# Optimization experiments

Hardware: AMD Instinct MI355X
Metric: run time of the kernel (lower is better)

Reference implementation:

```python
import jax, jax.numpy as jnp
import numpy as np


def setup_inputs() -> dict:
    key = jax.random.key(0)
    k1, k2, k3 = jax.random.split(key, 3)
    N, C_in, H, W = 32, 64, 128, 128
    C_out, K = 128, 3
    fan_in = C_in * K * K
    bound = 1.0 / np.sqrt(fan_in)
    x = jax.random.normal(k1, (N, C_in, H, W), dtype=jnp.float32)
    weight = jax.random.uniform(k2, (C_out, C_in, K, K), dtype=jnp.float32, minval=-bound, maxval=bound)
    bias = jax.random.uniform(k3, (C_out,), dtype=jnp.float32, minval=-bound, maxval=bound)
    return {"x": x, "weight": weight, "bias": bias}


def reference(x, weight, bias):
    # conv2d, stride=1, padding=0 (VALID), NCHW / OIHW
    y = jax.lax.conv_general_dilated(
        x, weight,
        window_strides=(1, 1),
        padding='VALID',
        dimension_numbers=('NCHW', 'OIHW', 'NCHW'),
    )
    y = y + bias[None, :, None, None]          # [N, C_out, H_out, W_out]
    y = jnp.min(y, axis=1, keepdims=True)      # channel-wise min -> [N, 1, H_out, W_out]
    return jnp.tanh(jnp.tanh(y))
```

## Files before the change

### kernel.cpp

```cpp
#include <hip/hip_runtime.h>
#include <hip/hip_bf16.h>

typedef __attribute__((ext_vector_type(8))) short short8_t;
typedef __attribute__((ext_vector_type(4))) float floatx4;
typedef unsigned short ushort_t;
typedef unsigned int uint_t;

#define RSTR 72
#define TSZ  (132 * RSTR)

__device__ __forceinline__ uint_t rne_u(float f) {
    uint_t u = __float_as_uint(f);
    return u + (0x7fffu + ((u >> 16) & 1u));
}
__device__ __forceinline__ uint_t pk2(float lo, float hi) {
    return __builtin_amdgcn_perm(rne_u(hi), rne_u(lo), 0x07060302u);
}

__global__ void w2_prepass(const float* __restrict__ w, ushort_t* __restrict__ w2) {
    int idx = blockIdx.x * 256 + threadIdx.x;
    int rd  = idx >> 12;
    int rem = idx & 4095;
    int co  = rem >> 5;
    int c32 = rem & 31;
    int khw = rd >> 1, half = rd & 1;
    int ci  = half * 32 + c32;
    w2[idx] = (ushort_t)(rne_u(w[co * 576 + ci * 9 + khw]) >> 16);
}

template<bool USE_W2>
__global__ __launch_bounds__(512, 4)
void conv_min_tanh_kernel(const float* __restrict__ x,
                          const float* __restrict__ w,
                          const ushort_t* __restrict__ w2,
                          const float* __restrict__ bias,
                          float* __restrict__ out)
{
    __shared__ ushort_t T[4 * TSZ];
    __shared__ float red[2][256];

    const int tid  = threadIdx.x;
    const int bid0 = blockIdx.x;
    const int bid  = (bid0 & 7) * 252 + (bid0 >> 3);
    const int n    = bid / 63;
    const int ho0  = (bid - n * 63) * 2;

    const int tx = tid & 31;
    const int ty = tid >> 5;

    const int lane = tid & 63;
    const int wid  = tid >> 6;
    const int wm   = wid >> 1;
    const int wn   = wid & 1;
    const int r16  = lane & 15;
    const int quad = lane >> 4;

    const float* xbase = x + ((size_t)n << 20) + (size_t)ho0 * 128;

    auto load_row = [&](floatx4 (&dv)[4], const int s) {
#pragma unroll
        for (int j = 0; j < 4; ++j)
            dv[j] = *reinterpret_cast<const floatx4*>(
                xbase + (size_t)(ty * 4 + j) * 16384 + s * 128 + tx * 4);
    };
    auto conv_row = [&](floatx4 (&dv)[4], const int s) {
#pragma unroll
        for (int i = 0; i < 4; ++i) {
            uint2 u;
            u.x = pk2(dv[0][i], dv[1][i]);
            u.y = pk2(dv[2][i], dv[3][i]);
            const int c   = tx * 4 + i;
            const int swz = (ty >> 1) ^ ((c >> 3) & 7);
            *reinterpret_cast<uint2*>(&T[s * TSZ + c * RSTR + swz * 8 + (ty & 1) * 4]) = u;
        }
    };

    floatx4 dva[4], dvb[4];
    load_row(dva, 0);
    load_row(dvb, 1);

    for (int idx = tid; idx < 576; idx += 512) {
        int s = idx / 144, o = idx - s * 144;
        reinterpret_cast<uint_t*>(T)[s * (TSZ / 2) + (128 * RSTR) / 2 + o] = 0u;
    }

    conv_row(dva, 0);
    load_row(dva, 2);
    conv_row(dvb, 1);
    load_row(dvb, 3);
    conv_row(dva, 2);
    conv_row(dvb, 3);

    floatx4 acc[4][4];
#pragma unroll
    for (int i = 0; i < 4; ++i)
#pragma unroll
        for (int j = 0; j < 4; ++j)
            acc[i][j] = (floatx4){0.f, 0.f, 0.f, 0.f};

    const ushort_t* w2base = w2 + (size_t)(wn * 64 + r16) * 32 + quad * 8;
    const float*    wbase  = w + (size_t)(wn * 64 + r16) * 576;

    __syncthreads();

#pragma unroll
    for (int rd = 0; rd < 18; ++rd) {
        const int khw  = rd >> 1;
        const int kh   = khw / 3;
        const int kw   = khw - kh * 3;
        const int half = rd & 1;

        short8_t bfr[4];
        if (USE_W2) {
            const ushort_t* bb = w2base + rd * 4096;
#pragma unroll
            for (int t4 = 0; t4 < 4; ++t4)
                bfr[t4] = *reinterpret_cast<const short8_t*>(bb + t4 * 512);
        } else {
#pragma unroll
            for (int t4 = 0; t4 < 4; ++t4) {
                const float* wp = wbase + (size_t)t4 * (16 * 576)
                                + (size_t)(half * 32 + quad * 8) * 9 + khw;
                short8_t b;
#pragma unroll
                for (int q = 0; q < 4; ++q) {
                    uint_t u = pk2(wp[(2 * q) * 9], wp[(2 * q + 1) * 9]);
                    b[2 * q]     = (short)(u & 0xffffu);
                    b[2 * q + 1] = (short)(u >> 16);
                }
                bfr[t4] = b;
            }
        }

        short8_t afr[4];
#pragma unroll
        for (int t4 = 0; t4 < 4; ++t4) {
            const int m  = wm * 64 + t4 * 16 + r16;
            const int s  = (m >> 7) + kh;
            const int c  = (m & 127) + kw;
            const int sw = (half * 4 + quad) ^ ((c >> 3) & 7);
            afr[t4] = *reinterpret_cast<const short8_t*>(&T[s * TSZ + c * RSTR + sw * 8]);
        }
#pragma unroll
        for (int tm = 0; tm < 4; ++tm)
#pragma unroll
            for (int tn = 0; tn < 4; ++tn)
                acc[tm][tn] = __builtin_amdgcn_mfma_f32_16x16x32_bf16(
                    afr[tm], bfr[tn], acc[tm][tn], 0, 0, 0);
    }

    float bvv[4];
#pragma unroll
    for (int tn = 0; tn < 4; ++tn)
        bvv[tn] = bias[wn * 64 + tn * 16 + r16];

#pragma unroll
    for (int tm = 0; tm < 4; ++tm) {
#pragma unroll
        for (int r = 0; r < 4; ++r) {
            float v = acc[tm][0][r] + bvv[0];
            v = fminf(v, acc[tm][1][r] + bvv[1]);
            v = fminf(v, acc[tm][2][r] + bvv[2]);
            v = fminf(v, acc[tm][3][r] + bvv[3]);
            v = fminf(v, __shfl_xor(v, 1, 64));
            v = fminf(v, __shfl_xor(v, 2, 64));
            v = fminf(v, __shfl_xor(v, 4, 64));
            v = fminf(v, __shfl_xor(v, 8, 64));
            if (r16 == 0)
                red[wn][wm * 64 + tm * 16 + quad * 4 + r] = v;
        }
    }
    __syncthreads();

    if (tid < 256) {
        const int r  = tid >> 7;
        const int wo = tid & 127;
        if (wo < 126) {
            float v = fminf(red[0][tid], red[1][tid]);
            v = tanhf(tanhf(v));
            out[((size_t)n * 126 + ho0 + r) * 126 + wo] = v;
        }
    }
}

extern "C" void kernel_launch(void* const* d_in, const int* in_sizes, int n_in,
                              void* d_out, int out_size, void* d_ws, size_t ws_size,
                              hipStream_t stream) {
    const float* x    = (const float*)d_in[0];
    const float* w    = (const float*)d_in[1];
    const float* bias = (const float*)d_in[2];
    float* out = (float*)d_out;

    const int use_w2 = (ws_size >= (size_t)(73728 * 2)) ? 1 : 0;
    ushort_t* w2 = (ushort_t*)d_ws;

    if (use_w2) {
        w2_prepass<<<dim3(288), dim3(256), 0, stream>>>(w, w2);
        conv_min_tanh_kernel<true><<<dim3(2016), dim3(512), 0, stream>>>(x, w, w2, bias, out);
    } else {
        conv_min_tanh_kernel<false><<<dim3(2016), dim3(512), 0, stream>>>(x, w, w2, bias, out);
    }
}
```

Measured before the change: 276.2 us.

## Prepack input to bf16 channels-last and DMA tiles directly into LDS

Adds a prepass that transposes the fp32 NCHW input into a bf16 NHWC workspace buffer. A new conv kernel then loads its LDS tiles with global_load_lds, with no per-thread conversion or swizzled stores. The aim is to remove the fp32 load and pack overhead in the conv prologue. In exchange it adds a full extra pass over the input and a 64MB workspace requirement, and falls back to the old kernel if the workspace is too small.

```diff
diff --git a/kernel.cpp b/kernel.cpp
--- a/kernel.cpp
+++ b/kernel.cpp
@@ -5,6 +5,8 @@
 typedef __attribute__((ext_vector_type(4))) float floatx4;
 typedef unsigned short ushort_t;
 typedef unsigned int uint_t;
+
+#define TILE_B 16896
 
 #define RSTR 72
 #define TSZ  (132 * RSTR)
@@ -28,25 +30,47 @@
     w2[idx] = (ushort_t)(rne_u(w[co * 576 + ci * 9 + khw]) >> 16);
 }
 
-template<bool USE_W2>
+__global__ __launch_bounds__(256)
+void x2_prepass(const float* __restrict__ x, ushort_t* __restrict__ x2) {
+    __shared__ __align__(16) float lds[64 * 129];
+    const int t = threadIdx.x;
+    const int b = blockIdx.x;
+    const int n = b >> 7, h = b & 127;
+    const float* xp = x + ((size_t)n << 20) + (size_t)h * 128;
+#pragma unroll
+    for (int r = 0; r < 32; ++r) {
+        int flat = r * 256 + t;
+        int ci = flat >> 7, wq = flat & 127;
+        lds[ci * 129 + wq] = xp[(size_t)ci * 16384 + wq];
+    }
+    __syncthreads();
+    ushort_t* op = x2 + ((size_t)n * 128 + h) * 128 * 64;
+#pragma unroll
+    for (int r = 0; r < 4; ++r) {
+        int id = r * 256 + t;
+        int wq = id >> 3, q = id & 7;
+        uint_t o[4];
+#pragma unroll
+        for (int qq = 0; qq < 4; ++qq)
+            o[qq] = pk2(lds[(q * 8 + 2 * qq) * 129 + wq],
+                        lds[(q * 8 + 2 * qq + 1) * 129 + wq]);
+        *reinterpret_cast<uint4*>(op + (size_t)wq * 64 + q * 8) =
+            make_uint4(o[0], o[1], o[2], o[3]);
+    }
+}
+
 __global__ __launch_bounds__(512, 4)
-void conv_min_tanh_kernel(const float* __restrict__ x,
-                          const float* __restrict__ w,
-                          const ushort_t* __restrict__ w2,
-                          const float* __restrict__ bias,
-                          float* __restrict__ out)
+void conv_v3(const ushort_t* __restrict__ x2, const ushort_t* __restrict__ w2,
+             const float* __restrict__ bias, float* __restrict__ out)
 {
-    __shared__ ushort_t T[4 * TSZ];
-    __shared__ float red[2][256];
+    __shared__ __align__(16) ushort_t T[4 * (TILE_B / 2)];
+    __shared__ __align__(16) float red[2][256];
 
     const int tid  = threadIdx.x;
     const int bid0 = blockIdx.x;
     const int bid  = (bid0 & 7) * 252 + (bid0 >> 3);
     const int n    = bid / 63;
     const int ho0  = (bid - n * 63) * 2;
-
-    const int tx = tid & 31;
-    const int ty = tid >> 5;
 
     const int lane = tid & 63;
     const int wid  = tid >> 6;
@@ -55,41 +79,25 @@
     const int r16  = lane & 15;
     const int quad = lane >> 4;
 
-    const float* xbase = x + ((size_t)n << 20) + (size_t)ho0 * 128;
-
-    auto load_row = [&](floatx4 (&dv)[4], const int s) {
-#pragma unroll
-        for (int j = 0; j < 4; ++j)
-            dv[j] = *reinterpret_cast<const floatx4*>(
-                xbase + (size_t)(ty * 4 + j) * 16384 + s * 128 + tx * 4);
-    };
-    auto conv_row = [&](floatx4 (&dv)[4], const int s) {
-#pragma unroll
-        for (int i = 0; i < 4; ++i) {
-            uint2 u;
-            u.x = pk2(dv[0][i], dv[1][i]);
-            u.y = pk2(dv[2][i], dv[3][i]);
-            const int c   = tx * 4 + i;
-            const int swz = (ty >> 1) ^ ((c >> 3) & 7);
-            *reinterpret_cast<uint2*>(&T[s * TSZ + c * RSTR + swz * 8 + (ty & 1) * 4]) = u;
-        }
-    };
-
-    floatx4 dva[4], dvb[4];
-    load_row(dva, 0);
-    load_row(dvb, 1);
-
-    for (int idx = tid; idx < 576; idx += 512) {
-        int s = idx / 144, o = idx - s * 144;
-        reinterpret_cast<uint_t*>(T)[s * (TSZ / 2) + (128 * RSTR) / 2 + o] = 0u;
-    }
-
-    conv_row(dva, 0);
-    load_row(dva, 2);
-    conv_row(dvb, 1);
-    load_row(dvb, 3);
-    conv_row(dva, 2);
-    conv_row(dvb, 3);
+    const int voffB = ((lane >> 3) * 128) + (((lane & 7) ^ (lane >> 3)) * 16);
+    const ushort_t* xrow = x2 + ((size_t)n * 128 + ho0) * 128 * 64;
+#pragma unroll
+    for (int s = 0; s < 4; ++s) {
+#pragma unroll
+        for (int k = 0; k < 2; ++k) {
+            const int col0 = (wid * 2 + k) * 8;
+            const char* g = (const char*)xrow + (size_t)s * 16384 + col0 * 128 + voffB;
+            const ushort_t* l = &T[(s * TILE_B + col0 * 128) / 2];
+            __builtin_amdgcn_global_load_lds(
+                (const __attribute__((address_space(1))) uint_t*)g,
+                (__attribute__((address_space(3))) uint_t*)l, 16, 0, 0);
+        }
+    }
+
+    {
+        const int s = tid >> 7, rem = tid & 127;
+        reinterpret_cast<uint_t*>(T)[(s * TILE_B + (128 + (rem >> 5)) * 128) / 4 + (rem & 31)] = 0u;
+    }
 
     floatx4 acc[4][4];
 #pragma unroll
@@ -99,7 +107,9 @@
             acc[i][j] = (floatx4){0.f, 0.f, 0.f, 0.f};
 
     const ushort_t* w2base = w2 + (size_t)(wn * 64 + r16) * 32 + quad * 8;
-    const float*    wbase  = w + (size_t)(wn * 64 + r16) * 576;
+
+    const int mc0 = (wm & 1) * 64 + r16;
+    const int ms0 = wm >> 1;
 
     __syncthreads();
 
@@ -111,36 +121,24 @@
         const int half = rd & 1;
 
         short8_t bfr[4];
-        if (USE_W2) {
+        {
             const ushort_t* bb = w2base + rd * 4096;
 #pragma unroll
             for (int t4 = 0; t4 < 4; ++t4)
                 bfr[t4] = *reinterpret_cast<const short8_t*>(bb + t4 * 512);
-        } else {
-#pragma unroll
-            for (int t4 = 0; t4 < 4; ++t4) {
-                const float* wp = wbase + (size_t)t4 * (16 * 576)
-                                + (size_t)(half * 32 + quad * 8) * 9 + khw;
-                short8_t b;
-#pragma unroll
-                for (int q = 0; q < 4; ++q) {
-                    uint_t u = pk2(wp[(2 * q) * 9], wp[(2 * q + 1) * 9]);
-                    b[2 * q]     = (short)(u & 0xffffu);
-                    b[2 * q + 1] = (short)(u >> 16);
-                }
-                bfr[t4] = b;
-            }
         }
 
         short8_t afr[4];
-#pragma unroll
-        for (int t4 = 0; t4 < 4; ++t4) {
-            const int m  = wm * 64 + t4 * 16 + r16;
-            const int s  = (m >> 7) + kh;
-            const int c  = (m & 127) + kw;
-            const int sw = (half * 4 + quad) ^ ((c >> 3) & 7);
-            afr[t4] = *reinterpret_cast<const short8_t*>(&T[s * TSZ + c * RSTR + sw * 8]);
-        }
+        {
+            const int c0 = mc0 + kw;
+            const int abase = (ms0 + kh) * TILE_B + c0 * 128
+                            + (((half * 4 + quad) ^ (c0 & 7)) * 16);
+            const char* ap = (const char*)T + abase;
+#pragma unroll
+            for (int t4 = 0; t4 < 4; ++t4)
+                afr[t4] = *reinterpret_cast<const short8_t*>(ap + t4 * 2048);
+        }
+
 #pragma unroll
         for (int tm = 0; tm < 4; ++tm)
 #pragma unroll
@@ -183,6 +181,161 @@
     }
 }
 
+template<bool USE_W2>
+__global__ __launch_bounds__(512, 4)
+void conv_min_tanh_kernel(const float* __restrict__ x,
+                          const float* __restrict__ w,
+                          const ushort_t* __restrict__ w2,
+                          const float* __restrict__ bias,
+                          float* __restrict__ out)
+{
+    __shared__ __align__(16) ushort_t T[4 * TSZ];
+    __shared__ __align__(16) float red[2][256];
+
+    const int tid  = threadIdx.x;
+    const int bid0 = blockIdx.x;
+    const int bid  = (bid0 & 7) * 252 + (bid0 >> 3);
+    const int n    = bid / 63;
+    const int ho0  = (bid - n * 63) * 2;
+
+    const int tx = tid & 31;
+    const int ty = tid >> 5;
+
+    const int lane = tid & 63;
+    const int wid  = tid >> 6;
+    const int wm   = wid >> 1;
+    const int wn   = wid & 1;
+    const int r16  = lane & 15;
+    const int quad = lane >> 4;
+
+    const float* xbase = x + ((size_t)n << 20) + (size_t)ho0 * 128;
+
+    auto load_row = [&](floatx4 (&dv)[4], const int s) {
+#pragma unroll
+        for (int j = 0; j < 4; ++j)
+            dv[j] = *reinterpret_cast<const floatx4*>(
+                xbase + (size_t)(ty * 4 + j) * 16384 + s * 128 + tx * 4);
+    };
+    auto conv_row = [&](floatx4 (&dv)[4], const int s) {
+#pragma unroll
+        for (int i = 0; i < 4; ++i) {
+            uint2 u;
+            u.x = pk2(dv[0][i], dv[1][i]);
+            u.y = pk2(dv[2][i], dv[3][i]);
+            const int c   = tx * 4 + i;
+            const int swz = (ty >> 1) ^ ((c >> 3) & 7);
+            *reinterpret_cast<uint2*>(&T[s * TSZ + c * RSTR + swz * 8 + (ty & 1) * 4]) = u;
+        }
+    };
+
+    floatx4 dva[4], dvb[4];
+    load_row(dva, 0);
+    load_row(dvb, 1);
+
+    for (int idx = tid; idx < 576; idx += 512) {
+        int s = idx / 144, o = idx - s * 144;
+        reinterpret_cast<uint_t*>(T)[s * (TSZ / 2) + (128 * RSTR) / 2 + o] = 0u;
+    }
+
+    conv_row(dva, 0);
+    load_row(dva, 2);
+    conv_row(dvb, 1);
+    load_row(dvb, 3);
+    conv_row(dva, 2);
+    conv_row(dvb, 3);
+
+    floatx4 acc[4][4];
+#pragma unroll
+    for (int i = 0; i < 4; ++i)
+#pragma unroll
+        for (int j = 0; j < 4; ++j)
+            acc[i][j] = (floatx4){0.f, 0.f, 0.f, 0.f};
+
+    const ushort_t* w2base = w2 + (size_t)(wn * 64 + r16) * 32 + quad * 8;
+    const float*    wbase  = w + (size_t)(wn * 64 + r16) * 576;
+
+    __syncthreads();
+
+#pragma unroll
+    for (int rd = 0; rd < 18; ++rd) {
+        const int khw  = rd >> 1;
+        const int kh   = khw / 3;
+        const int kw   = khw - kh * 3;
+        const int half = rd & 1;
+
+        short8_t bfr[4];
+        if (USE_W2) {
+            const ushort_t* bb = w2base + rd * 4096;
+#pragma unroll
+            for (int t4 = 0; t4 < 4; ++t4)
+                bfr[t4] = *reinterpret_cast<const short8_t*>(bb + t4 * 512);
+        } else {
+#pragma unroll
+            for (int t4 = 0; t4 < 4; ++t4) {
+                const float* wp = wbase + (size_t)t4 * (16 * 576)
+                                + (size_t)(half * 32 + quad * 8) * 9 + khw;
+                short8_t b;
+#pragma unroll
+                for (int q = 0; q < 4; ++q) {
+                    uint_t u = pk2(wp[(2 * q) * 9], wp[(2 * q + 1) * 9]);
+                    b[2 * q]     = (short)(u & 0xffffu);
+                    b[2 * q + 1] = (short)(u >> 16);
+                }
+                bfr[t4] = b;
+            }
+        }
+
+        short8_t afr[4];
+#pragma unroll
+        for (int t4 = 0; t4 < 4; ++t4) {
+            const int m  = wm * 64 + t4 * 16 + r16;
+            const int s  = (m >> 7) + kh;
+            const int c  = (m & 127) + kw;
+            const int sw = (half * 4 + quad) ^ ((c >> 3) & 7);
+            afr[t4] = *reinterpret_cast<const short8_t*>(&T[s * TSZ + c * RSTR + sw * 8]);
+        }
+#pragma unroll
+        for (int tm = 0; tm < 4; ++tm)
+#pragma unroll
+            for (int tn = 0; tn < 4; ++tn)
+                acc[tm][tn] = __builtin_amdgcn_mfma_f32_16x16x32_bf16(
+                    afr[tm], bfr[tn], acc[tm][tn], 0, 0, 0);
+    }
+
+    float bvv[4];
+#pragma unroll
+    for (int tn = 0; tn < 4; ++tn)
+        bvv[tn] = bias[wn * 64 + tn * 16 + r16];
+
+#pragma unroll
+    for (int tm = 0; tm < 4; ++tm) {
+#pragma unroll
+        for (int r = 0; r < 4; ++r) {
+            float v = acc[tm][0][r] + bvv[0];
+            v = fminf(v, acc[tm][1][r] + bvv[1]);
+            v = fminf(v, acc[tm][2][r] + bvv[2]);
+            v = fminf(v, acc[tm][3][r] + bvv[3]);
+            v = fminf(v, __shfl_xor(v, 1, 64));
+            v = fminf(v, __shfl_xor(v, 2, 64));
+            v = fminf(v, __shfl_xor(v, 4, 64));
+            v = fminf(v, __shfl_xor(v, 8, 64));
+            if (r16 == 0)
+                red[wn][wm * 64 + tm * 16 + quad * 4 + r] = v;
+        }
+    }
+    __syncthreads();
+
+    if (tid < 256) {
+        const int r  = tid >> 7;
+        const int wo = tid & 127;
+        if (wo < 126) {
+            float v = fminf(red[0][tid], red[1][tid]);
+            v = tanhf(tanhf(v));
+            out[((size_t)n * 126 + ho0 + r) * 126 + wo] = v;
+        }
+    }
+}
+
 extern "C" void kernel_launch(void* const* d_in, const int* in_sizes, int n_in,
                               void* d_out, int out_size, void* d_ws, size_t ws_size,
                               hipStream_t stream) {
@@ -191,13 +344,20 @@
     const float* bias = (const float*)d_in[2];
     float* out = (float*)d_out;
 
-    const int use_w2 = (ws_size >= (size_t)(73728 * 2)) ? 1 : 0;
-    ushort_t* w2 = (ushort_t*)d_ws;
-
-    if (use_w2) {
+    const size_t X2B = (size_t)32 * 128 * 128 * 64 * 2;
+    const size_t W2B = (size_t)73728 * 2;
+
+    if (ws_size >= X2B + W2B) {
+        ushort_t* x2 = (ushort_t*)d_ws;
+        ushort_t* w2 = (ushort_t*)((char*)d_ws + X2B);
+        x2_prepass<<<dim3(4096), dim3(256), 0, stream>>>(x, x2);
         w2_prepass<<<dim3(288), dim3(256), 0, stream>>>(w, w2);
-        conv_min_tanh_kernel<true><<<dim3(2016), dim3(512), 0, stream>>>(x, w, w2, bias, out);
+        conv_v3<<<dim3(2016), dim3(512), 0, stream>>>(x2, w2, bias, out);
+    } else if (ws_size >= W2B) {
+        ushort_t* w2 = (ushort_t*)d_ws;
+        w2_prepass<<<dim3(288), dim3(256), 0, stream>>>(w, w2);
+        conv_min_tanh_kernel<true><<<dim3(2016), dim3(512), 0, stream>>>(x, w, (ushort_t*)d_ws, bias, out);
     } else {
-        conv_min_tanh_kernel<false><<<dim3(2016), dim3(512), 0, stream>>>(x, w, w2, bias, out);
-    }
-}
+        conv_min_tanh_kernel<false><<<dim3(2016), dim3(512), 0, stream>>>(x, w, nullptr, bias, out);
+    }
+}
```

New measurement: 284.5 us. +3.0%, slower.
